# Kernel optimization log

Hardware: AMD Instinct MI355X
Metric: run time of the kernel (lower is better)

Reference implementation:

```python
import jax, jax.numpy as jnp
import numpy as np

N, M, D, O, H = 32768, 64, 8, 4, 4  # n_points, inducing, in_size, out_size, n_hypers
JITTER = 1e-4


def vec2tril(vec, m):
    idx = jnp.tril_indices(m)
    out = jnp.zeros((*vec.shape[:-1], m, m), vec.dtype)
    return out.at[..., idx[0], idx[1]].set(vec)


def _sqdist(a, b):
    # a: [..., Na, D], b: [..., Nb, D] -> [..., Na, Nb]
    return ((a ** 2).sum(-1)[..., :, None] + (b ** 2).sum(-1)[..., None, :]
            - 2.0 * jnp.einsum('...nd,...md->...nm', a, b))


def setup_inputs() -> dict:
    key = jax.random.key(0)
    ks = jax.random.split(key, 5)
    x = jax.random.normal(ks[0], (N, D), dtype=jnp.float32)
    z = jax.random.normal(ks[1], (O, M, D), dtype=jnp.float32)
    u_mean = 0.5 * jax.random.normal(ks[2], (O, M, 1), dtype=jnp.float32)
    u_tril_vec = jnp.ones((O, M * (M + 1) // 2), dtype=jnp.float32)
    log_ls = 0.1 * jax.random.normal(ks[3], (H, O, D), dtype=jnp.float32)
    log_var = 0.1 * jax.random.normal(ks[4], (H, O), dtype=jnp.float32)
    return {"x": x, "z": z, "u_mean": u_mean, "u_tril_vec": u_tril_vec,
            "log_ls": log_ls, "log_var": log_var}


def reference(x, z, u_mean, u_tril_vec, log_ls, log_var):
    h, o, m = log_ls.shape[0], z.shape[0], z.shape[1]
    n = x.shape[0]
    ls = jnp.exp(log_ls)      # [H,O,D] ARD lengthscales (sampled hypers)
    var = jnp.exp(log_var)    # [H,O]  signal variance
    xs = x[None, None, :, :] / ls[:, :, None, :]   # [H,O,N,D]
    zs = z[None, :, :, :] / ls[:, :, None, :]      # [H,O,M,D]
    kfu = var[:, :, None, None] * jnp.exp(-0.5 * _sqdist(xs, zs))  # [H,O,N,M]
    kuu = var[:, :, None, None] * jnp.exp(-0.5 * _sqdist(zs, zs))  # [H,O,M,M]
    kuf = jnp.swapaxes(kfu, -1, -2)                                # [H,O,M,N]
    Lkuu = jnp.linalg.cholesky(kuu + JITTER * jnp.eye(m, dtype=x.dtype))
    solve = jax.scipy.linalg.solve_triangular
    LKinvu = solve(Lkuu, jnp.broadcast_to(u_mean, (h, o, m, 1)), lower=True)
    LKinvKuf = solve(Lkuu, kuf, lower=True)                        # [H,O,M,N]
    kff_diag = jnp.broadcast_to(var[:, :, None], (h, o, n))
    diag1 = (LKinvKuf ** 2).sum(-2)                                # [H,O,N]
    u_tril = vec2tril(u_tril_vec, m)                               # [O,M,M]
    # NOTE: torch.triangular_solve default upper=True -> uses triu(Lkuu);
    # replicated faithfully with lower=False.
    LKinvLs = solve(Lkuu, jnp.broadcast_to(u_tril, (h, o, m, m)), lower=False)
    vec2 = jnp.einsum('...ij,...ik->...jk', LKinvLs, LKinvKuf)     # [H,O,M,N]
    diag2 = (vec2 ** 2).sum(-2)
    pred_mu = jnp.einsum('...ij,...ik->...jk', LKinvKuf, LKinvu)[..., 0]  # [H,O,N]
    pred_var = kff_diag - diag1 + diag2
    return pred_mu, pred_var
```

## Files before the change

kernel.cpp:

```cpp
#include <hip/hip_runtime.h>
#include <math.h>

#define N_PTS 32768
#define MM 64
#define DD 8
#define OO 4
#define HH 4
#define NPAIR 16
#define JITTERV 1e-4
#define LOG2E 1.4426950408889634

#define ES_OFF 0
#define W_OFF 4096
#define ZT_OFF (4096 + 64)
#define CC_OFF (ZT_OFF + 512)
#define INV2_OFF (CC_OFF + 64)
#define VAR_OFF (INV2_OFF + 8)
#define PAIR_STRIDE 4752

__global__ __launch_bounds__(256) void setup_kernel(
    const float* __restrict__ z, const float* __restrict__ u_mean,
    const float* __restrict__ utv, const float* __restrict__ log_ls,
    const float* __restrict__ log_var, float* __restrict__ ws)
{
    const int p = blockIdx.x;
    const int h = p / OO, o = p % OO;
    const int tid = threadIdx.x;
    const int r = tid & 63;
    const int q = tid >> 6;

    __shared__ double A[64][65];
    __shared__ double Mi[64][65];
    __shared__ double Pm[64][65];
    __shared__ double Us[64][65];
    __shared__ double zsh[64][9];
    __shared__ double ils[8];
    __shared__ double piv[64];
    __shared__ double idg[64];
    __shared__ double yv[64];

    const float* ll = log_ls + (h * OO + o) * DD;
    const double lv = (double)log_var[h * OO + o];
    const double var = exp(lv);

    if (tid < DD) ils[tid] = exp(-(double)ll[tid]);
    __syncthreads();

    if (tid < 64) {
        #pragma unroll
        for (int d = 0; d < DD; ++d)
            zsh[tid][d] = (double)z[(o * MM + tid) * DD + d] * ils[d];
    }
    __syncthreads();

    #pragma unroll
    for (int jj = 0; jj < 16; ++jj) {
        const int j = q * 16 + jj;
        double s = 0;
        #pragma unroll
        for (int d = 0; d < DD; ++d) { double df = zsh[r][d] - zsh[j][d]; s += df * df; }
        A[r][j] = var * exp(-0.5 * s) + ((r == j) ? (double)JITTERV : 0.0);
    }
    __syncthreads();

    for (int k = 0; k < 64; ++k) {
        const double pk = A[k][k];
        const double ipk = 1.0 / pk;
        if (tid == 0) piv[k] = pk;
        const double cf = A[r][k] * ipk;
        #pragma unroll
        for (int jj = 0; jj < 16; ++jj) {
            const int j = q * 16 + jj;
            if (j > k && j <= r) A[r][j] -= cf * A[j][k];
        }
        __syncthreads();
    }

    if (tid < 64) idg[tid] = 1.0 / sqrt(piv[tid]);
    __syncthreads();

    #pragma unroll
    for (int jj = 0; jj < 16; ++jj) {
        const int j = q * 16 + jj;
        if (j <= r) A[r][j] *= idg[j];
    }
    for (int e = tid; e < 64 * 64; e += 256) Mi[e >> 6][e & 63] = 0.0;
    __syncthreads();

    if (tid < 64) {
        const int j = tid;
        double y[64];
        #pragma unroll
        for (int t = 0; t < 64; ++t) y[t] = (t == j) ? idg[j] : 0.0;
        #pragma unroll
        for (int i = 1; i < 64; ++i) {
            double s0 = 0, s1 = 0, s2 = 0, s3 = 0;
            #pragma unroll
            for (int t = 0; t < i; t += 4) {
                s0 += A[i][t] * y[t];
                if (t + 1 < i) s1 += A[i][t + 1] * y[t + 1];
                if (t + 2 < i) s2 += A[i][t + 2] * y[t + 2];
                if (t + 3 < i) s3 += A[i][t + 3] * y[t + 3];
            }
            const double yi = -idg[i] * ((s0 + s1) + (s2 + s3));
            y[i] = (i > j) ? yi : y[i];
        }
        #pragma unroll
        for (int i = 0; i < 64; ++i) Mi[i][j] = y[i];
    }

    {
        const float* uo = utv + o * (MM * (MM + 1) / 2);
        for (int e = tid; e < 64 * 64; e += 256) {
            const int i = e >> 6, a = e & 63;
            Us[i][a] = (a <= i) ? (double)uo[i * (i + 1) / 2 + a] * idg[i] : 0.0;
        }
    }
    __syncthreads();

    if (tid < 64) {
        double s0 = 0, s1 = 0;
        #pragma unroll 16
        for (int t = 0; t < 64; t += 2) {
            s0 += Mi[tid][t] * (double)u_mean[o * MM + t];
            s1 += Mi[tid][t + 1] * (double)u_mean[o * MM + t + 1];
        }
        yv[tid] = s0 + s1;
    }
    __syncthreads();

    float* wsp = ws + (size_t)p * PAIR_STRIDE;

    if (tid < 64) {
        double s0 = 0, s1 = 0;
        #pragma unroll 16
        for (int i = 0; i < 64; i += 2) {
            s0 += Mi[i][tid] * yv[i];
            s1 += Mi[i + 1][tid] * yv[i + 1];
        }
        wsp[W_OFF + tid] = (float)(s0 + s1);
    }

    #pragma unroll
    for (int aa = 0; aa < 16; ++aa) {
        const int a = q * 16 + aa;
        double s0 = 0, s1 = 0;
        #pragma unroll 16
        for (int i = 0; i < 64; i += 2) {
            s0 += Us[i][a] * Mi[i][r];
            s1 += Us[i + 1][a] * Mi[i + 1][r];
        }
        Pm[a][r] = s0 + s1;
    }
    __syncthreads();

    #pragma unroll
    for (int rr = 0; rr < 16; ++rr) {
        const int row = q * 16 + rr;
        double s0 = 0, s1 = 0;
        #pragma unroll 16
        for (int t = 0; t < 64; ++t) {
            s0 += Pm[t][row] * Pm[t][r];
            s1 += Mi[t][row] * Mi[t][r];
        }
        const double s = s0 - s1;
        float v;
        if (r < row) v = 0.f;
        else if (r == row) v = (float)(0.5 * s);
        else v = (float)s;
        wsp[ES_OFF + row * 64 + r] = v;
    }

    if (tid < 64) {
        const int m = tid;
        double B = 0;
        #pragma unroll
        for (int d = 0; d < DD; ++d) {
            const double zv = (double)z[(o * MM + m) * DD + d];
            const double zt = zv * ils[d] * ils[d];
            wsp[ZT_OFF + m * DD + d] = (float)(zt * LOG2E);
            B += zv * zt;
        }
        wsp[CC_OFF + m] = (float)((lv - 0.5 * B) * LOG2E);
    }
    if (tid < DD) wsp[INV2_OFF + tid] = (float)(ils[tid] * ils[tid] * LOG2E);
    if (tid == 0) wsp[VAR_OFF] = (float)var;
}

__global__ __launch_bounds__(256) void predict_kernel(
    const float* __restrict__ x, const float* __restrict__ ws,
    float* __restrict__ out)
{
    const int p = blockIdx.y;
    const float* __restrict__ wsp = ws + (size_t)p * PAIR_STRIDE;

    __shared__ float s_Es[4096];
    __shared__ float s_zt[512];
    __shared__ float s_cc[64];
    __shared__ float s_wv[64];
    __shared__ float s_iv2[8];
    __shared__ float s_var;

    const int tid = threadIdx.x;
    {
        const float4* __restrict__ Ev = (const float4*)(wsp + ES_OFF);
        float4* sv = (float4*)s_Es;
        #pragma unroll
        for (int e = 0; e < 4; ++e) sv[tid + e * 256] = Ev[tid + e * 256];
    }
    s_zt[tid] = wsp[ZT_OFF + tid];
    s_zt[tid + 256] = wsp[ZT_OFF + tid + 256];
    if (tid < 64) { s_cc[tid] = wsp[CC_OFF + tid]; s_wv[tid] = wsp[W_OFF + tid]; }
    if (tid < 8) s_iv2[tid] = wsp[INV2_OFF + tid];
    if (tid == 0) s_var = wsp[VAR_OFF];
    __syncthreads();

    const int n = blockIdx.x * 256 + tid;

    float4 xa = *(const float4*)(x + n * 8);
    float4 xb = *(const float4*)(x + n * 8 + 4);
    float xd[8] = {xa.x, xa.y, xa.z, xa.w, xb.x, xb.y, xb.z, xb.w};

    float Aq = 0.f;
    #pragma unroll
    for (int d = 0; d < 8; ++d) Aq = fmaf(xd[d] * xd[d], s_iv2[d], Aq);
    const float a0 = -0.5f * Aq;

    float k[64];
    #pragma unroll
    for (int m = 0; m < 64; ++m) {
        float s = s_cc[m] + a0;
        #pragma unroll
        for (int d = 0; d < 8; ++d) s = fmaf(xd[d], s_zt[m * 8 + d], s);
        k[m] = exp2f(s);
    }

    float mu = 0.f;
    #pragma unroll
    for (int m = 0; m < 64; ++m) mu = fmaf(k[m], s_wv[m], mu);

    float acc = 0.f;
    #pragma unroll
    for (int i = 0; i < 64; ++i) {
        float s = 0.f;
        #pragma unroll
        for (int j = (i & ~3); j < 64; j += 4) {
            float4 e = *(const float4*)(s_Es + i * 64 + j);
            s = fmaf(e.x, k[j], s);
            s = fmaf(e.y, k[j + 1], s);
            s = fmaf(e.z, k[j + 2], s);
            s = fmaf(e.w, k[j + 3], s);
        }
        acc = fmaf(k[i], s, acc);
    }

    out[p * N_PTS + n] = mu;
    out[NPAIR * N_PTS + p * N_PTS + n] = s_var + 2.0f * acc;
}

extern "C" void kernel_launch(void* const* d_in, const int* in_sizes, int n_in,
                              void* d_out, int out_size, void* d_ws, size_t ws_size,
                              hipStream_t stream) {
    const float* x   = (const float*)d_in[0];
    const float* z   = (const float*)d_in[1];
    const float* um  = (const float*)d_in[2];
    const float* utv = (const float*)d_in[3];
    const float* lls = (const float*)d_in[4];
    const float* lvr = (const float*)d_in[5];
    float* ws = (float*)d_ws;
    float* out = (float*)d_out;

    setup_kernel<<<16, 256, 0, stream>>>(z, um, utv, lls, lvr, ws);
    predict_kernel<<<dim3(N_PTS / 256, NPAIR), 256, 0, stream>>>(x, ws, out);
}
```

Measured before the change: 245.3 us.

## Block triangular inverse, split E-matrix build into kernel, two points per thread

The serial 64-thread triangular inversion becomes a 16x16 diagonal-block inversion followed by level-wise block updates that use all 256 threads. The final double-precision E-matrix product moves out of the 16-block setup kernel into a separate kernel over 64 blocks, with intermediates passed through global workspace. The predict kernel now handles two points per thread so shared-memory loads of E and z are reused across both. The costs are an extra kernel launch, a global round trip for the intermediates, and higher register pressure in predict that may lower occupancy.

Result: faster. 211.6 us (-13.7%).

```diff
diff --git a/kernel.cpp b/kernel.cpp
--- a/kernel.cpp
+++ b/kernel.cpp
@@ -17,8 +17,10 @@
 #define INV2_OFF (CC_OFF + 64)
 #define VAR_OFF (INV2_OFF + 8)
 #define PAIR_STRIDE 4752
-
-__global__ __launch_bounds__(256) void setup_kernel(
+#define F64_BASE_D 38016
+#define PMMI_STRIDE_D 8192
+
+__global__ __launch_bounds__(256) void setup_chol(
     const float* __restrict__ z, const float* __restrict__ u_mean,
     const float* __restrict__ utv, const float* __restrict__ log_ls,
     const float* __restrict__ log_var, float* __restrict__ ws)
@@ -31,7 +33,6 @@
 
     __shared__ double A[64][65];
     __shared__ double Mi[64][65];
-    __shared__ double Pm[64][65];
     __shared__ double Us[64][65];
     __shared__ double zsh[64][9];
     __shared__ double ils[8];
@@ -88,25 +89,51 @@
     __syncthreads();
 
     if (tid < 64) {
-        const int j = tid;
-        double y[64];
-        #pragma unroll
-        for (int t = 0; t < 64; ++t) y[t] = (t == j) ? idg[j] : 0.0;
-        #pragma unroll
-        for (int i = 1; i < 64; ++i) {
-            double s0 = 0, s1 = 0, s2 = 0, s3 = 0;
+        const int b = tid >> 4, c = tid & 15;
+        const int g0 = b * 16;
+        double y[16];
+        #pragma unroll
+        for (int t = 0; t < 16; ++t) y[t] = (t == c) ? idg[g0 + c] : 0.0;
+        #pragma unroll
+        for (int i = 1; i < 16; ++i) {
+            double s = 0;
             #pragma unroll
-            for (int t = 0; t < i; t += 4) {
-                s0 += A[i][t] * y[t];
-                if (t + 1 < i) s1 += A[i][t + 1] * y[t + 1];
-                if (t + 2 < i) s2 += A[i][t + 2] * y[t + 2];
-                if (t + 3 < i) s3 += A[i][t + 3] * y[t + 3];
+            for (int t = 0; t < i; ++t) s += A[g0 + i][g0 + t] * y[t];
+            const double yi = -idg[g0 + i] * s;
+            y[i] = (i > c) ? yi : y[i];
+        }
+        #pragma unroll
+        for (int i = 0; i < 16; ++i) Mi[g0 + i][g0 + c] = y[i];
+    }
+    __syncthreads();
+
+    {
+        const int lr = tid >> 4, lc = tid & 15;
+        #pragma unroll
+        for (int lev = 1; lev < 4; ++lev) {
+            #pragma unroll
+            for (int bb = 0; bb < 4 - lev; ++bb) {
+                const int i = bb + lev, j = bb;
+                double s = 0;
+                #pragma unroll
+                for (int k = j; k < i; ++k)
+                    #pragma unroll
+                    for (int t = 0; t < 16; ++t)
+                        s += A[i * 16 + lr][k * 16 + t] * Mi[k * 16 + t][j * 16 + lc];
+                Us[bb * 16 + lr][lc] = s;
             }
-            const double yi = -idg[i] * ((s0 + s1) + (s2 + s3));
-            y[i] = (i > j) ? yi : y[i];
-        }
-        #pragma unroll
-        for (int i = 0; i < 64; ++i) Mi[i][j] = y[i];
+            __syncthreads();
+            #pragma unroll
+            for (int bb = 0; bb < 4 - lev; ++bb) {
+                const int i = bb + lev, j = bb;
+                double s = 0;
+                #pragma unroll
+                for (int t = 0; t < 16; ++t)
+                    s += Mi[i * 16 + lr][i * 16 + t] * Us[bb * 16 + t][lc];
+                Mi[i * 16 + lr][j * 16 + lc] = -s;
+            }
+            __syncthreads();
+        }
     }
 
     {
@@ -116,8 +143,6 @@
             Us[i][a] = (a <= i) ? (double)uo[i * (i + 1) / 2 + a] * idg[i] : 0.0;
         }
     }
-    __syncthreads();
-
     if (tid < 64) {
         double s0 = 0, s1 = 0;
         #pragma unroll 16
@@ -130,6 +155,9 @@
     __syncthreads();
 
     float* wsp = ws + (size_t)p * PAIR_STRIDE;
+    double* ws64 = (double*)ws;
+    double* pm64 = ws64 + F64_BASE_D + (size_t)p * PMMI_STRIDE_D;
+    double* mi64 = pm64 + 4096;
 
     if (tid < 64) {
         double s0 = 0, s1 = 0;
@@ -150,26 +178,9 @@
             s0 += Us[i][a] * Mi[i][r];
             s1 += Us[i + 1][a] * Mi[i + 1][r];
         }
-        Pm[a][r] = s0 + s1;
-    }
-    __syncthreads();
-
-    #pragma unroll
-    for (int rr = 0; rr < 16; ++rr) {
-        const int row = q * 16 + rr;
-        double s0 = 0, s1 = 0;
-        #pragma unroll 16
-        for (int t = 0; t < 64; ++t) {
-            s0 += Pm[t][row] * Pm[t][r];
-            s1 += Mi[t][row] * Mi[t][r];
-        }
-        const double s = s0 - s1;
-        float v;
-        if (r < row) v = 0.f;
-        else if (r == row) v = (float)(0.5 * s);
-        else v = (float)s;
-        wsp[ES_OFF + row * 64 + r] = v;
-    }
+        pm64[a * 64 + r] = s0 + s1;
+    }
+    for (int e = tid; e < 4096; e += 256) mi64[e] = Mi[e >> 6][e & 63];
 
     if (tid < 64) {
         const int m = tid;
@@ -185,6 +196,53 @@
     }
     if (tid < DD) wsp[INV2_OFF + tid] = (float)(ils[tid] * ils[tid] * LOG2E);
     if (tid == 0) wsp[VAR_OFF] = (float)var;
+}
+
+__global__ __launch_bounds__(256) void e_kernel(float* __restrict__ ws)
+{
+    const int p = blockIdx.y;
+    const int cx = blockIdx.x;
+    const int tid = threadIdx.x;
+    const int c = tid & 63, rr = tid >> 6;
+
+    __shared__ double sPm[64][64];
+    __shared__ double sMi[64][64];
+
+    const double* ws64 = (const double*)ws;
+    const double* pm64 = ws64 + F64_BASE_D + (size_t)p * PMMI_STRIDE_D;
+    const double* mi64 = pm64 + 4096;
+
+    {
+        const double2* gp = (const double2*)pm64;
+        const double2* gm = (const double2*)mi64;
+        double2* sp = (double2*)&sPm[0][0];
+        double2* sm = (double2*)&sMi[0][0];
+        #pragma unroll
+        for (int e = 0; e < 8; ++e) {
+            sp[tid + e * 256] = gp[tid + e * 256];
+            sm[tid + e * 256] = gm[tid + e * 256];
+        }
+    }
+    __syncthreads();
+
+    float* esp = ws + (size_t)p * PAIR_STRIDE + ES_OFF;
+
+    #pragma unroll
+    for (int ii = 0; ii < 4; ++ii) {
+        const int row = cx * 16 + rr * 4 + ii;
+        double s0 = 0, s1 = 0;
+        #pragma unroll 16
+        for (int t = 0; t < 64; ++t) {
+            s0 += sPm[t][row] * sPm[t][c];
+            s1 += sMi[t][row] * sMi[t][c];
+        }
+        const double s = s0 - s1;
+        float v;
+        if (c < row) v = 0.f;
+        else if (c == row) v = (float)(0.5 * s);
+        else v = (float)s;
+        esp[row * 64 + c] = v;
+    }
 }
 
 __global__ __launch_bounds__(256) void predict_kernel(
@@ -215,47 +273,73 @@
     if (tid == 0) s_var = wsp[VAR_OFF];
     __syncthreads();
 
-    const int n = blockIdx.x * 256 + tid;
-
-    float4 xa = *(const float4*)(x + n * 8);
-    float4 xb = *(const float4*)(x + n * 8 + 4);
-    float xd[8] = {xa.x, xa.y, xa.z, xa.w, xb.x, xb.y, xb.z, xb.w};
-
-    float Aq = 0.f;
-    #pragma unroll
-    for (int d = 0; d < 8; ++d) Aq = fmaf(xd[d] * xd[d], s_iv2[d], Aq);
-    const float a0 = -0.5f * Aq;
-
-    float k[64];
+    const int nA = blockIdx.x * 512 + tid;
+    const int nB = nA + 256;
+
+    float4 xa = *(const float4*)(x + nA * 8);
+    float4 xb = *(const float4*)(x + nA * 8 + 4);
+    float xdA[8] = {xa.x, xa.y, xa.z, xa.w, xb.x, xb.y, xb.z, xb.w};
+    float4 xc = *(const float4*)(x + nB * 8);
+    float4 xe = *(const float4*)(x + nB * 8 + 4);
+    float xdB[8] = {xc.x, xc.y, xc.z, xc.w, xe.x, xe.y, xe.z, xe.w};
+
+    float iv[8];
+    #pragma unroll
+    for (int d = 0; d < 8; ++d) iv[d] = s_iv2[d];
+
+    float AqA = 0.f, AqB = 0.f;
+    #pragma unroll
+    for (int d = 0; d < 8; ++d) {
+        AqA = fmaf(xdA[d] * xdA[d], iv[d], AqA);
+        AqB = fmaf(xdB[d] * xdB[d], iv[d], AqB);
+    }
+    const float a0A = -0.5f * AqA;
+    const float a0B = -0.5f * AqB;
+
+    float kA[64], kB[64];
+    float muA = 0.f, muB = 0.f;
     #pragma unroll
     for (int m = 0; m < 64; ++m) {
-        float s = s_cc[m] + a0;
-        #pragma unroll
-        for (int d = 0; d < 8; ++d) s = fmaf(xd[d], s_zt[m * 8 + d], s);
-        k[m] = exp2f(s);
-    }
-
-    float mu = 0.f;
-    #pragma unroll
-    for (int m = 0; m < 64; ++m) mu = fmaf(k[m], s_wv[m], mu);
-
-    float acc = 0.f;
+        float4 z0 = *(const float4*)(s_zt + m * 8);
+        float4 z1 = *(const float4*)(s_zt + m * 8 + 4);
+        const float cc = s_cc[m];
+        float sA = cc + a0A, sB = cc + a0B;
+        sA = fmaf(xdA[0], z0.x, sA); sB = fmaf(xdB[0], z0.x, sB);
+        sA = fmaf(xdA[1], z0.y, sA); sB = fmaf(xdB[1], z0.y, sB);
+        sA = fmaf(xdA[2], z0.z, sA); sB = fmaf(xdB[2], z0.z, sB);
+        sA = fmaf(xdA[3], z0.w, sA); sB = fmaf(xdB[3], z0.w, sB);
+        sA = fmaf(xdA[4], z1.x, sA); sB = fmaf(xdB[4], z1.x, sB);
+        sA = fmaf(xdA[5], z1.y, sA); sB = fmaf(xdB[5], z1.y, sB);
+        sA = fmaf(xdA[6], z1.z, sA); sB = fmaf(xdB[6], z1.z, sB);
+        sA = fmaf(xdA[7], z1.w, sA); sB = fmaf(xdB[7], z1.w, sB);
+        kA[m] = exp2f(sA);
+        kB[m] = exp2f(sB);
+        const float wv = s_wv[m];
+        muA = fmaf(kA[m], wv, muA);
+        muB = fmaf(kB[m], wv, muB);
+    }
+
+    float accA = 0.f, accB = 0.f;
     #pragma unroll
     for (int i = 0; i < 64; ++i) {
-        float s = 0.f;
+        float sA = 0.f, sB = 0.f;
         #pragma unroll
         for (int j = (i & ~3); j < 64; j += 4) {
             float4 e = *(const float4*)(s_Es + i * 64 + j);
-            s = fmaf(e.x, k[j], s);
-            s = fmaf(e.y, k[j + 1], s);
-            s = fmaf(e.z, k[j + 2], s);
-            s = fmaf(e.w, k[j + 3], s);
-        }
-        acc = fmaf(k[i], s, acc);
-    }
-
-    out[p * N_PTS + n] = mu;
-    out[NPAIR * N_PTS + p * N_PTS + n] = s_var + 2.0f * acc;
+            sA = fmaf(e.x, kA[j], sA);     sB = fmaf(e.x, kB[j], sB);
+            sA = fmaf(e.y, kA[j + 1], sA); sB = fmaf(e.y, kB[j + 1], sB);
+            sA = fmaf(e.z, kA[j + 2], sA); sB = fmaf(e.z, kB[j + 2], sB);
+            sA = fmaf(e.w, kA[j + 3], sA); sB = fmaf(e.w, kB[j + 3], sB);
+        }
+        accA = fmaf(kA[i], sA, accA);
+        accB = fmaf(kB[i], sB, accB);
+    }
+
+    const float varf = s_var;
+    out[p * N_PTS + nA] = muA;
+    out[p * N_PTS + nB] = muB;
+    out[NPAIR * N_PTS + p * N_PTS + nA] = varf + 2.0f * accA;
+    out[NPAIR * N_PTS + p * N_PTS + nB] = varf + 2.0f * accB;
 }
 
 extern "C" void kernel_launch(void* const* d_in, const int* in_sizes, int n_in,
@@ -270,6 +354,7 @@
     float* ws = (float*)d_ws;
     float* out = (float*)d_out;
 
-    setup_kernel<<<16, 256, 0, stream>>>(z, um, utv, lls, lvr, ws);
-    predict_kernel<<<dim3(N_PTS / 256, NPAIR), 256, 0, stream>>>(x, ws, out);
+    setup_chol<<<16, 256, 0, stream>>>(z, um, utv, lls, lvr, ws);
+    e_kernel<<<dim3(4, NPAIR), 256, 0, stream>>>(ws);
+    predict_kernel<<<dim3(N_PTS / 512, NPAIR), 256, 0, stream>>>(x, ws, out);
 }
```
